# Kernel tuning notes

Measured on AMD Instinct MI355X. Metric: run time of the kernel, lower is better.

## Reference

```python
import jax, jax.numpy as jnp
import numpy as np

B, H, S, D = 4, 16, 2048, 64  # head_dim = num_dims // num_heads = 1024 // 16


def setup_inputs() -> dict:
    key = jax.random.key(0)
    kq, kk, kv = jax.random.split(key, 3)
    q = jax.random.normal(kq, (B, H, S, D), dtype=jnp.float32)
    k = jax.random.normal(kk, (B, H, S, D), dtype=jnp.float32)
    v = jax.random.normal(kv, (B, H, S, D), dtype=jnp.float32)
    return {"q": q, "k": k, "v": v}


def reference(q, k, v):
    # scores = (q @ k^T) / sqrt(head_dim)  -> [B, H, S, S]
    scale = 1.0 / np.sqrt(D).astype(np.float32)
    scores = jnp.einsum("bhqd,bhkd->bhqk", q, k) * scale
    # softmax over keys; dropout rate is 0.0 (eval), so it's the identity
    weights = jax.nn.softmax(scores, axis=-1)
    # weights @ v -> [B, H, S, D]
    return jnp.einsum("bhqk,bhkd->bhqd", weights, v)
```

## Files before the change

kernel.cpp:

```cpp
#include <hip/hip_runtime.h>
#include <hip/hip_bf16.h>

#define S_LEN 2048
#define BH_TOTAL 64
#define D_DIM 64
#define NT2 16

typedef float f32x4 __attribute__((ext_vector_type(4)));
typedef float f32x16 __attribute__((ext_vector_type(16)));
typedef __bf16 bf16x8 __attribute__((ext_vector_type(8)));
typedef unsigned short u16x8 __attribute__((ext_vector_type(8)));
typedef unsigned int u32;
typedef u32 u32x2 __attribute__((ext_vector_type(2)));
typedef u32 u32x4 __attribute__((ext_vector_type(4)));

union BF8 { u32x4 w; u16x8 u; bf16x8 b; };

#if __has_builtin(__builtin_amdgcn_exp2f)
#define EX2(x) __builtin_amdgcn_exp2f(x)
#else
#define EX2(x) exp2f(x)
#endif

__device__ __forceinline__ unsigned short f2b(float f) {
  __bf16 h = (__bf16)f;
  return __builtin_bit_cast(unsigned short, h);
}
__device__ __forceinline__ u32 pk2(float a, float b) {
  return (u32)f2b(a) | ((u32)f2b(b) << 16);
}

__device__ __forceinline__ u32x2 pl32(u32 x, u32 y) {
#if __has_builtin(__builtin_amdgcn_permlane32_swap)
  return __builtin_amdgcn_permlane32_swap(x, y, false, false);
#else
  u32 xs = (u32)__shfl_xor((int)x, 32);
  u32 ys = (u32)__shfl_xor((int)y, 32);
  int hi = (int)(threadIdx.x & 32);
  u32x2 r;
  r.x = hi ? ys : x;
  r.y = hi ? y : xs;
  return r;
#endif
}

__device__ __forceinline__ void gload16(const unsigned short* g, unsigned short* l) {
  __builtin_amdgcn_global_load_lds(
      (const __attribute__((address_space(1))) unsigned int*)g,
      (__attribute__((address_space(3))) unsigned int*)l, 16, 0, 0);
}

__global__ __launch_bounds__(256)
void prep(const float* __restrict__ K, const float* __restrict__ V,
          unsigned short* __restrict__ Kb, unsigned short* __restrict__ Vt) {
  __shared__ unsigned short T[64][72];
  if (blockIdx.x < 4096) {
    int i = blockIdx.x * 256 + threadIdx.x;
    const f32x4* src = (const f32x4*)K;
    f32x4 a = src[2 * i], b = src[2 * i + 1];
    u16x8 o;
    #pragma unroll
    for (int j = 0; j < 4; ++j) { o[j] = f2b(a[j]); o[j + 4] = f2b(b[j]); }
    ((u16x8*)Kb)[i] = o;
  } else {
    int bid = blockIdx.x - 4096;
    int bh = bid >> 5, t5 = bid & 31;
    int s0 = t5 * 64;
    int tid = threadIdx.x;
    {
      int s = tid >> 2, d0 = (tid & 3) * 16;
      const float* src = V + ((size_t)bh * S_LEN + s0 + s) * D_DIM + d0;
      #pragma unroll
      for (int j = 0; j < 16; j += 4) {
        f32x4 x = *(const f32x4*)(src + j);
        #pragma unroll
        for (int q2 = 0; q2 < 4; ++q2) T[d0 + j + q2][s] = f2b(x[q2]);
      }
    }
    __syncthreads();
    {
      int d = tid >> 2, c0 = (tid & 3) * 16;
      unsigned short* dst = Vt + ((size_t)bh * D_DIM + d) * S_LEN + s0 + c0;
      u16x8 o;
      #pragma unroll
      for (int q2 = 0; q2 < 8; ++q2) o[q2] = T[d][c0 + q2];
      *(u16x8*)dst = o;
      #pragma unroll
      for (int q2 = 0; q2 < 8; ++q2) o[q2] = T[d][c0 + 8 + q2];
      *(u16x8*)(dst + 8) = o;
    }
  }
}

__device__ __forceinline__ void exppack(const f32x16 sv, float& ls, BF8& pA, BF8& pB) {
  u32 wlo[4], whi[4];
  #pragma unroll
  for (int b2 = 0; b2 < 4; ++b2) {
    float e0 = EX2(sv[4 * b2 + 0]), e1 = EX2(sv[4 * b2 + 1]);
    float e2 = EX2(sv[4 * b2 + 2]), e3 = EX2(sv[4 * b2 + 3]);
    ls += (e0 + e1) + (e2 + e3);
    wlo[b2] = pk2(e0, e1);
    whi[b2] = pk2(e2, e3);
  }
  u32x2 rlo = pl32(wlo[0], wlo[1]);
  u32x2 rhi = pl32(whi[0], whi[1]);
  pA.w[0] = rlo.x; pA.w[1] = rhi.x; pA.w[2] = rlo.y; pA.w[3] = rhi.y;
  rlo = pl32(wlo[2], wlo[3]);
  rhi = pl32(whi[2], whi[3]);
  pB.w[0] = rlo.x; pB.w[1] = rhi.x; pB.w[2] = rlo.y; pB.w[3] = rhi.y;
}

#define MFMA32(A, B, C) __builtin_amdgcn_mfma_f32_32x32x16_bf16((A), (B), (C), 0, 0, 0)

__global__ __launch_bounds__(512, 4)
void attn_fwd(const float* __restrict__ Q, const unsigned short* __restrict__ Kb,
              const unsigned short* __restrict__ Vt, float* __restrict__ O) {
  const int wg = blockIdx.x;
  const int id = (wg & 7) * 64 + (wg >> 3);
  const int qt = id & 7;
  const int bh = id >> 3;

  const int tid = threadIdx.x;
  const int w = tid >> 6;
  const int ln = tid & 63;
  const int l31 = ln & 31;
  const int h = ln >> 5;

  __shared__ __align__(16) unsigned short Ks[2][2][4096];
  __shared__ __align__(16) unsigned short Vs[2][2][4096];

  const size_t hbase = (size_t)bh * S_LEN * D_DIM;
  const unsigned short* Kh = Kb + hbase;
  const unsigned short* Vh = Vt + hbase;

  const int q0 = qt * 256 + w * 32;

  BF8 qf[4];
  {
    const float sc = 0.125f * 1.44269504088896f;
    const float* qp = Q + hbase + (size_t)(q0 + l31) * D_DIM + h * 8;
    #pragma unroll
    for (int f = 0; f < 4; ++f) {
      f32x4 a = *(const f32x4*)(qp + f * 16);
      f32x4 b = *(const f32x4*)(qp + f * 16 + 4);
      #pragma unroll
      for (int j = 0; j < 4; ++j) {
        qf[f].u[j]     = f2b(a[j] * sc);
        qf[f].u[j + 4] = f2b(b[j] * sc);
      }
    }
  }

  const int srow = ln >> 3;
  const int scol = ((ln & 7) ^ srow) * 8;
  const unsigned short* kbase = Kh + (size_t)(w * 8 + srow) * D_DIM + scol;
  const unsigned short* vbase = Vh + (size_t)(w * 8 + srow) * S_LEN + scol;

  const int swz = (ln & 7) << 4;
  const int rb = l31 * 128;
  int cx[4];
  #pragma unroll
  for (int m = 0; m < 4; ++m) cx[m] = (m * 32 + h * 16) ^ swz;

  f32x16 oa0, oa1;
  #pragma unroll
  for (int j = 0; j < 16; ++j) { oa0[j] = 0.f; oa1[j] = 0.f; }
  float ls = 0.f;

  gload16(kbase,        &Ks[0][0][w * 512]);
  gload16(kbase + 4096, &Ks[0][1][w * 512]);
  gload16(vbase,        &Vs[0][0][w * 512]);
  gload16(vbase + 64,   &Vs[0][1][w * 512]);
  __syncthreads();

  for (int t = 0; t < NT2; ++t) {
    const int cur = t & 1;
    if (t + 1 < NT2) {
      const unsigned short* kp = kbase + (size_t)(t + 1) * 8192;
      const unsigned short* vp = vbase + (t + 1) * 128;
      gload16(kp,        &Ks[cur ^ 1][0][w * 512]);
      gload16(kp + 4096, &Ks[cur ^ 1][1][w * 512]);
      gload16(vp,        &Vs[cur ^ 1][0][w * 512]);
      gload16(vp + 64,   &Vs[cur ^ 1][1][w * 512]);
    }

    #pragma unroll
    for (int c = 0; c < 2; ++c) {
      const char* KsB = (const char*)&Ks[cur][c][0];
      const char* VsB = (const char*)&Vs[cur][c][0];

      f32x16 s0, s1;
      #pragma unroll
      for (int j = 0; j < 16; ++j) { s0[j] = 0.f; s1[j] = 0.f; }
      __builtin_amdgcn_s_setprio(1);
      #pragma unroll
      for (int f = 0; f < 4; ++f) {
        BF8 k0, k1;
        k0.u = *(const u16x8*)(KsB + rb + cx[f]);
        k1.u = *(const u16x8*)(KsB + 4096 + rb + cx[f]);
        s0 = MFMA32(k0.b, qf[f].b, s0);
        s1 = MFMA32(k1.b, qf[f].b, s1);
      }
      __builtin_amdgcn_s_setprio(0);

      BF8 va, vb, vc, vd;
      va.u = *(const u16x8*)(VsB + rb + cx[0]);
      vb.u = *(const u16x8*)(VsB + 4096 + rb + cx[0]);
      vc.u = *(const u16x8*)(VsB + rb + cx[1]);
      vd.u = *(const u16x8*)(VsB + 4096 + rb + cx[1]);

      BF8 pf0, pf1, pf2, pf3;
      exppack(s0, ls, pf0, pf1);
      exppack(s1, ls, pf2, pf3);

      __builtin_amdgcn_s_setprio(1);
      oa0 = MFMA32(va.b, pf0.b, oa0);
      oa1 = MFMA32(vb.b, pf0.b, oa1);
      va.u = *(const u16x8*)(VsB + rb + cx[2]);
      vb.u = *(const u16x8*)(VsB + 4096 + rb + cx[2]);
      oa0 = MFMA32(vc.b, pf1.b, oa0);
      oa1 = MFMA32(vd.b, pf1.b, oa1);
      vc.u = *(const u16x8*)(VsB + rb + cx[3]);
      vd.u = *(const u16x8*)(VsB + 4096 + rb + cx[3]);
      oa0 = MFMA32(va.b, pf2.b, oa0);
      oa1 = MFMA32(vb.b, pf2.b, oa1);
      oa0 = MFMA32(vc.b, pf3.b, oa0);
      oa1 = MFMA32(vd.b, pf3.b, oa1);
      __builtin_amdgcn_s_setprio(0);
    }

    __syncthreads();
  }

  {
    float lo2 = __shfl_xor(ls, 32);
    float inv = 1.0f / (ls + lo2);
    float* op = O + hbase + (size_t)(q0 + l31) * D_DIM;
    #pragma unroll
    for (int dt = 0; dt < 2; ++dt) {
      const f32x16 oa = dt ? oa1 : oa0;
      #pragma unroll
      for (int b2 = 0; b2 < 4; ++b2) {
        f32x4 vv;
        vv[0] = oa[4 * b2 + 0] * inv;
        vv[1] = oa[4 * b2 + 1] * inv;
        vv[2] = oa[4 * b2 + 2] * inv;
        vv[3] = oa[4 * b2 + 3] * inv;
        *(f32x4*)(op + dt * 32 + b2 * 8 + h * 4) = vv;
      }
    }
  }
}

extern "C" void kernel_launch(void* const* d_in, const int* in_sizes, int n_in,
                              void* d_out, int out_size, void* d_ws, size_t ws_size,
                              hipStream_t stream) {
  const float* q = (const float*)d_in[0];
  const float* k = (const float*)d_in[1];
  const float* v = (const float*)d_in[2];
  float* o = (float*)d_out;
  unsigned short* kb = (unsigned short*)d_ws;
  unsigned short* vt = kb + (size_t)BH_TOTAL * S_LEN * D_DIM;

  prep<<<dim3(4096 + 2048), 256, 0, stream>>>(k, v, kb, vt);
  attn_fwd<<<dim3(512), 512, 0, stream>>>(q, kb, vt, o);
}
```

Measured before the change: 106.3 us.

## Give each wave two 32-row query tiles to reuse K/V fragments

Halves the workgroup to 4 waves (256 threads), with each wave processing 64 query rows as two 32-row sub-tiles. Every K and V fragment read from LDS now feeds two MFMAs, which halves LDS traffic per unit of math. The K/V tile per iteration shrinks to 64 keys, so there are 32 iterations and half the shared memory. The cost is roughly doubled accumulator and score registers per wave and fewer waves per block to hide latency.

```diff
diff --git a/kernel.cpp b/kernel.cpp
--- a/kernel.cpp
+++ b/kernel.cpp
@@ -4,7 +4,7 @@
 #define S_LEN 2048
 #define BH_TOTAL 64
 #define D_DIM 64
-#define NT2 16
+#define NT 32
 
 typedef float f32x4 __attribute__((ext_vector_type(4)));
 typedef float f32x16 __attribute__((ext_vector_type(16)));
@@ -112,7 +112,7 @@
 
 #define MFMA32(A, B, C) __builtin_amdgcn_mfma_f32_32x32x16_bf16((A), (B), (C), 0, 0, 0)
 
-__global__ __launch_bounds__(512, 4)
+__global__ __launch_bounds__(256, 2)
 void attn_fwd(const float* __restrict__ Q, const unsigned short* __restrict__ Kb,
               const unsigned short* __restrict__ Vt, float* __restrict__ O) {
   const int wg = blockIdx.x;
@@ -126,35 +126,39 @@
   const int l31 = ln & 31;
   const int h = ln >> 5;
 
-  __shared__ __align__(16) unsigned short Ks[2][2][4096];
-  __shared__ __align__(16) unsigned short Vs[2][2][4096];
+  __shared__ __align__(16) unsigned short Ks[2][4096];
+  __shared__ __align__(16) unsigned short Vs[2][4096];
 
   const size_t hbase = (size_t)bh * S_LEN * D_DIM;
   const unsigned short* Kh = Kb + hbase;
   const unsigned short* Vh = Vt + hbase;
 
-  const int q0 = qt * 256 + w * 32;
-
-  BF8 qf[4];
+  const int q0 = qt * 256 + w * 64;
+
+  BF8 qf0[4], qf1[4];
   {
     const float sc = 0.125f * 1.44269504088896f;
-    const float* qp = Q + hbase + (size_t)(q0 + l31) * D_DIM + h * 8;
-    #pragma unroll
-    for (int f = 0; f < 4; ++f) {
-      f32x4 a = *(const f32x4*)(qp + f * 16);
-      f32x4 b = *(const f32x4*)(qp + f * 16 + 4);
-      #pragma unroll
-      for (int j = 0; j < 4; ++j) {
-        qf[f].u[j]     = f2b(a[j] * sc);
-        qf[f].u[j + 4] = f2b(b[j] * sc);
+    #pragma unroll
+    for (int qs = 0; qs < 2; ++qs) {
+      const float* qp = Q + hbase + (size_t)(q0 + qs * 32 + l31) * D_DIM + h * 8;
+      #pragma unroll
+      for (int f = 0; f < 4; ++f) {
+        f32x4 a = *(const f32x4*)(qp + f * 16);
+        f32x4 b = *(const f32x4*)(qp + f * 16 + 4);
+        BF8& dst = qs ? qf1[f] : qf0[f];
+        #pragma unroll
+        for (int j = 0; j < 4; ++j) {
+          dst.u[j]     = f2b(a[j] * sc);
+          dst.u[j + 4] = f2b(b[j] * sc);
+        }
       }
     }
   }
 
   const int srow = ln >> 3;
   const int scol = ((ln & 7) ^ srow) * 8;
-  const unsigned short* kbase = Kh + (size_t)(w * 8 + srow) * D_DIM + scol;
-  const unsigned short* vbase = Vh + (size_t)(w * 8 + srow) * S_LEN + scol;
+  const unsigned short* ks0 = Kh + (size_t)(w * 16 + srow) * D_DIM + scol;
+  const unsigned short* vs0 = Vh + (size_t)(w * 16 + srow) * S_LEN + scol;
 
   const int swz = (ln & 7) << 4;
   const int rb = l31 * 128;
@@ -162,83 +166,97 @@
   #pragma unroll
   for (int m = 0; m < 4; ++m) cx[m] = (m * 32 + h * 16) ^ swz;
 
-  f32x16 oa0, oa1;
-  #pragma unroll
-  for (int j = 0; j < 16; ++j) { oa0[j] = 0.f; oa1[j] = 0.f; }
-  float ls = 0.f;
-
-  gload16(kbase,        &Ks[0][0][w * 512]);
-  gload16(kbase + 4096, &Ks[0][1][w * 512]);
-  gload16(vbase,        &Vs[0][0][w * 512]);
-  gload16(vbase + 64,   &Vs[0][1][w * 512]);
+  f32x16 oa00, oa01, oa10, oa11;
+  #pragma unroll
+  for (int j = 0; j < 16; ++j) { oa00[j] = 0.f; oa01[j] = 0.f; oa10[j] = 0.f; oa11[j] = 0.f; }
+  float ls0 = 0.f, ls1 = 0.f;
+
+  gload16(ks0,             &Ks[0][w * 1024]);
+  gload16(ks0 + 512,       &Ks[0][w * 1024 + 512]);
+  gload16(vs0,             &Vs[0][w * 1024]);
+  gload16(vs0 + 8 * S_LEN, &Vs[0][w * 1024 + 512]);
   __syncthreads();
 
-  for (int t = 0; t < NT2; ++t) {
+  for (int t = 0; t < NT; ++t) {
     const int cur = t & 1;
-    if (t + 1 < NT2) {
-      const unsigned short* kp = kbase + (size_t)(t + 1) * 8192;
-      const unsigned short* vp = vbase + (t + 1) * 128;
-      gload16(kp,        &Ks[cur ^ 1][0][w * 512]);
-      gload16(kp + 4096, &Ks[cur ^ 1][1][w * 512]);
-      gload16(vp,        &Vs[cur ^ 1][0][w * 512]);
-      gload16(vp + 64,   &Vs[cur ^ 1][1][w * 512]);
-    }
-
-    #pragma unroll
-    for (int c = 0; c < 2; ++c) {
-      const char* KsB = (const char*)&Ks[cur][c][0];
-      const char* VsB = (const char*)&Vs[cur][c][0];
-
-      f32x16 s0, s1;
-      #pragma unroll
-      for (int j = 0; j < 16; ++j) { s0[j] = 0.f; s1[j] = 0.f; }
-      __builtin_amdgcn_s_setprio(1);
-      #pragma unroll
-      for (int f = 0; f < 4; ++f) {
-        BF8 k0, k1;
-        k0.u = *(const u16x8*)(KsB + rb + cx[f]);
-        k1.u = *(const u16x8*)(KsB + 4096 + rb + cx[f]);
-        s0 = MFMA32(k0.b, qf[f].b, s0);
-        s1 = MFMA32(k1.b, qf[f].b, s1);
-      }
-      __builtin_amdgcn_s_setprio(0);
-
-      BF8 va, vb, vc, vd;
-      va.u = *(const u16x8*)(VsB + rb + cx[0]);
-      vb.u = *(const u16x8*)(VsB + 4096 + rb + cx[0]);
+    if (t + 1 < NT) {
+      const unsigned short* kp = ks0 + (size_t)(t + 1) * 4096;
+      const unsigned short* vp = vs0 + (t + 1) * 64;
+      gload16(kp,             &Ks[cur ^ 1][w * 1024]);
+      gload16(kp + 512,       &Ks[cur ^ 1][w * 1024 + 512]);
+      gload16(vp,             &Vs[cur ^ 1][w * 1024]);
+      gload16(vp + 8 * S_LEN, &Vs[cur ^ 1][w * 1024 + 512]);
+    }
+
+    const char* KsB = (const char*)&Ks[cur][0];
+    const char* VsB = (const char*)&Vs[cur][0];
+
+    f32x16 s00, s01, s10, s11;
+    #pragma unroll
+    for (int j = 0; j < 16; ++j) { s00[j] = 0.f; s01[j] = 0.f; s10[j] = 0.f; s11[j] = 0.f; }
+    __builtin_amdgcn_s_setprio(1);
+    #pragma unroll
+    for (int f = 0; f < 4; ++f) {
+      BF8 k0, k1;
+      k0.u = *(const u16x8*)(KsB + rb + cx[f]);
+      k1.u = *(const u16x8*)(KsB + 4096 + rb + cx[f]);
+      s00 = MFMA32(k0.b, qf0[f].b, s00);
+      s01 = MFMA32(k1.b, qf0[f].b, s01);
+      s10 = MFMA32(k0.b, qf1[f].b, s10);
+      s11 = MFMA32(k1.b, qf1[f].b, s11);
+    }
+    __builtin_amdgcn_s_setprio(0);
+
+    BF8 va, vb;
+    va.u = *(const u16x8*)(VsB + rb + cx[0]);
+    vb.u = *(const u16x8*)(VsB + 4096 + rb + cx[0]);
+
+    BF8 p00A, p00B, p01A, p01B, p10A, p10B, p11A, p11B;
+    exppack(s00, ls0, p00A, p00B);
+    exppack(s01, ls0, p01A, p01B);
+    exppack(s10, ls1, p10A, p10B);
+    exppack(s11, ls1, p11A, p11B);
+
+    __builtin_amdgcn_s_setprio(1);
+    {
+      BF8 vc, vd;
       vc.u = *(const u16x8*)(VsB + rb + cx[1]);
       vd.u = *(const u16x8*)(VsB + 4096 + rb + cx[1]);
-
-      BF8 pf0, pf1, pf2, pf3;
-      exppack(s0, ls, pf0, pf1);
-      exppack(s1, ls, pf2, pf3);
-
-      __builtin_amdgcn_s_setprio(1);
-      oa0 = MFMA32(va.b, pf0.b, oa0);
-      oa1 = MFMA32(vb.b, pf0.b, oa1);
+      oa00 = MFMA32(va.b, p00A.b, oa00);
+      oa01 = MFMA32(vb.b, p00A.b, oa01);
+      oa10 = MFMA32(va.b, p10A.b, oa10);
+      oa11 = MFMA32(vb.b, p10A.b, oa11);
       va.u = *(const u16x8*)(VsB + rb + cx[2]);
       vb.u = *(const u16x8*)(VsB + 4096 + rb + cx[2]);
-      oa0 = MFMA32(vc.b, pf1.b, oa0);
-      oa1 = MFMA32(vd.b, pf1.b, oa1);
+      oa00 = MFMA32(vc.b, p00B.b, oa00);
+      oa01 = MFMA32(vd.b, p00B.b, oa01);
+      oa10 = MFMA32(vc.b, p10B.b, oa10);
+      oa11 = MFMA32(vd.b, p10B.b, oa11);
       vc.u = *(const u16x8*)(VsB + rb + cx[3]);
       vd.u = *(const u16x8*)(VsB + 4096 + rb + cx[3]);
-      oa0 = MFMA32(va.b, pf2.b, oa0);
-      oa1 = MFMA32(vb.b, pf2.b, oa1);
-      oa0 = MFMA32(vc.b, pf3.b, oa0);
-      oa1 = MFMA32(vd.b, pf3.b, oa1);
-      __builtin_amdgcn_s_setprio(0);
-    }
+      oa00 = MFMA32(va.b, p01A.b, oa00);
+      oa01 = MFMA32(vb.b, p01A.b, oa01);
+      oa10 = MFMA32(va.b, p11A.b, oa10);
+      oa11 = MFMA32(vb.b, p11A.b, oa11);
+      oa00 = MFMA32(vc.b, p01B.b, oa00);
+      oa01 = MFMA32(vd.b, p01B.b, oa01);
+      oa10 = MFMA32(vc.b, p11B.b, oa10);
+      oa11 = MFMA32(vd.b, p11B.b, oa11);
+    }
+    __builtin_amdgcn_s_setprio(0);
 
     __syncthreads();
   }
 
-  {
-    float lo2 = __shfl_xor(ls, 32);
-    float inv = 1.0f / (ls + lo2);
-    float* op = O + hbase + (size_t)(q0 + l31) * D_DIM;
+  #pragma unroll
+  for (int qs = 0; qs < 2; ++qs) {
+    float lsq = qs ? ls1 : ls0;
+    float lo2 = __shfl_xor(lsq, 32);
+    float inv = 1.0f / (lsq + lo2);
+    float* op = O + hbase + (size_t)(q0 + qs * 32 + l31) * D_DIM;
     #pragma unroll
     for (int dt = 0; dt < 2; ++dt) {
-      const f32x16 oa = dt ? oa1 : oa0;
+      const f32x16 oa = qs ? (dt ? oa11 : oa10) : (dt ? oa01 : oa00);
       #pragma unroll
       for (int b2 = 0; b2 < 4; ++b2) {
         f32x4 vv;
@@ -263,5 +281,5 @@
   unsigned short* vt = kb + (size_t)BH_TOTAL * S_LEN * D_DIM;
 
   prep<<<dim3(4096 + 2048), 256, 0, stream>>>(k, v, kb, vt);
-  attn_fwd<<<dim3(512), 512, 0, stream>>>(q, kb, vt, o);
-}
+  attn_fwd<<<dim3(512), 256, 0, stream>>>(q, kb, vt, o);
+}
```

Result: slower. 108.4 us (+2.0%).
